# Optimization experiments

Measured on AMD Instinct MI355X. Metric: run time of the kernel, lower is better.

## Reference

```python
import jax, jax.numpy as jnp
import numpy as np

N_LAYERS = 3
HIDDEN = 128
N_NODES = 50000
N_EDGES = 800000
NEG_SLOPE = 0.2  # PyG GATConv default negative_slope
EPS = 1e-16      # PyG softmax denominator eps


def setup_inputs() -> dict:
    key = jax.random.key(0)
    ks = jax.random.split(key, 6)
    z = jax.random.normal(ks[0], (N_NODES, HIDDEN), dtype=jnp.float32)
    edge_index = jax.random.randint(ks[1], (2, N_EDGES), 0, N_NODES, dtype=jnp.int32)
    scale = 1.0 / np.sqrt(HIDDEN)
    Ws = jax.random.normal(ks[2], (N_LAYERS, HIDDEN, HIDDEN), dtype=jnp.float32) * scale
    a_src = jax.random.normal(ks[3], (N_LAYERS, HIDDEN), dtype=jnp.float32) * scale
    a_dst = jax.random.normal(ks[4], (N_LAYERS, HIDDEN), dtype=jnp.float32) * scale
    bias = jnp.zeros((N_LAYERS, HIDDEN), dtype=jnp.float32)
    return {"z": z, "edge_index": edge_index, "Ws": Ws, "a_src": a_src,
            "a_dst": a_dst, "bias": bias}


def _gat_conv(h, W, a_s, a_d, b, src, dst):
    # Linear transform: [N, D]
    x = h @ W
    # Per-node attention logits, gathered per edge
    alpha_s = x @ a_s  # [N]
    alpha_d = x @ a_d  # [N]
    e = jax.nn.leaky_relu(alpha_s[src] + alpha_d[dst], NEG_SLOPE)  # [E]
    # Segment softmax over incoming edges of each destination node
    e_max = jax.ops.segment_max(e, dst, num_segments=N_NODES)
    ex = jnp.exp(e - e_max[dst])
    denom = jax.ops.segment_sum(ex, dst, num_segments=N_NODES)
    alpha = ex / (denom[dst] + EPS)  # [E]
    # Weighted scatter-aggregation of source features
    out = jax.ops.segment_sum(x[src] * alpha[:, None], dst, num_segments=N_NODES)
    return out + b


def reference(z, edge_index, Ws, a_src, a_dst, bias):
    # add_self_loops=True (PyG GATConv default)
    loop = jnp.arange(N_NODES, dtype=edge_index.dtype)
    src = jnp.concatenate([edge_index[0], loop])
    dst = jnp.concatenate([edge_index[1], loop])
    h = z
    for l in range(N_LAYERS):
        h = _gat_conv(h, Ws[l], a_src[l], a_dst[l], bias[l], src, dst)
        if l < N_LAYERS - 1:
            h = jax.nn.relu(h)
    return h
```

## Files before the change

### kernel.cpp

```cpp
#include <hip/hip_runtime.h>

#define NN 50000
#define HID 128
#define NE 800000
#define ET (NE + NN)
#define NEG_SLOPE 0.2f
#define CAP 64

typedef __attribute__((ext_vector_type(8))) short short8v;
typedef __attribute__((ext_vector_type(4))) float f32x4;

__device__ inline float b2f(unsigned short u) {
    union { unsigned int i; float f; } x; x.i = ((unsigned int)u) << 16; return x.f;
}
__device__ inline unsigned short f2b(float f) {
    unsigned int x; __builtin_memcpy(&x, &f, 4);
    unsigned int lsb = (x >> 16) & 1u;
    x += 0x7fffu + lsb;
    return (unsigned short)(x >> 16);
}
__device__ inline void splitbf(float v, unsigned short& hi, unsigned short& lo) {
    hi = f2b(v);
    lo = f2b(v - b2f(hi));
}

__global__ void probe_dtype(const unsigned short* __restrict__ z, int* __restrict__ flag) {
    int lane = threadIdx.x;
    unsigned short a = z[lane * 4];
    unsigned short b = z[lane * 4 + 2];
    int ea = (a >> 7) & 0xFF, eb = (b >> 7) & 0xFF;
    int w1 = (ea >= 0x9A || (ea <= 0x30 && a != 0)) ? 1 : 0;
    int w2 = (eb >= 0x9A || (eb <= 0x30 && b != 0)) ? 1 : 0;
    int wild = __popcll(__ballot(w1)) + __popcll(__ballot(w2));
    if (lane == 0) *flag = (wild < 8) ? 1 : 0;
}

__global__ void cvt3(const void* __restrict__ a, const void* __restrict__ b,
                     const void* __restrict__ c, float* __restrict__ oa,
                     float* __restrict__ ob, float* __restrict__ oc,
                     const int* __restrict__ flag) {
    int i = blockIdx.x * 256 + threadIdx.x;
    if (i >= 3 * 3 * HID) return;
    int which = i / (3 * HID), j = i - which * (3 * HID);
    const void* in = which == 0 ? a : which == 1 ? b : c;
    float* out = which == 0 ? oa : which == 1 ? ob : oc;
    out[j] = *flag ? b2f(((const unsigned short*)in)[j]) : ((const float*)in)[j];
}

__global__ void wprep(const void* __restrict__ Ws, unsigned short* __restrict__ Wb,
                      const int* __restrict__ flag) {
    int i = blockIdx.x * 256 + threadIdx.x;
    if (i >= 3 * HID * HID) return;
    int L = i >> 14;
    int k = (i >> 7) & 127;
    int n = i & 127;
    float v = *flag ? b2f(((const unsigned short*)Ws)[i]) : ((const float*)Ws)[i];
    unsigned short hi, lo;
    splitbf(v, hi, lo);
    unsigned short* hbase = Wb + (size_t)L * 2 * HID * HID;
    unsigned short* lbase = hbase + HID * HID;
    int bo = (n * 256 + k * 2) ^ ((n & 7) << 4);
    *(unsigned short*)((char*)hbase + bo) = hi;
    lbase[n * HID + k] = lo;
}

#define SCHUNK 1024
__global__ __launch_bounds__(256) void scatter_padded(
        const int* __restrict__ ei, int* __restrict__ pos, int* __restrict__ csr) {
    const int rng  = blockIdx.x & 7;
    const int base = (blockIdx.x >> 3) * SCHUNK;
#pragma unroll
    for (int k = 0; k < SCHUNK / 256; ++k) {
        int e = base + k * 256 + threadIdx.x;
        if (e >= ET) continue;
        int d = (e < NE) ? ei[NE + e] : (e - NE);
        if ((d * 8) / NN != rng) continue;
        int s = (e < NE) ? ei[e] : d;
        int slot = atomicAdd(&pos[d], 1);
        if (slot < CAP) csr[(d << 6) + slot] = s;
    }
}

__global__ __launch_bounds__(256) void gemm_alpha(
        const void* __restrict__ h_, const unsigned short* __restrict__ Wb,
        const float* __restrict__ a_s, const float* __restrict__ a_d,
        unsigned short* __restrict__ x, float* __restrict__ alpha_s, float* __restrict__ alpha_d,
        const int* __restrict__ flag) {
    __shared__ unsigned short Wh[HID * HID];
    const int t = threadIdx.x;
    const int base = blockIdx.x * 64;
    const int hf = *flag;
    const unsigned short* Wlo = Wb + HID * HID;

#pragma unroll
    for (int i = 0; i < 8; ++i) {
        int c = i * 256 + t;
        ((short8v*)Wh)[c] = ((const short8v*)Wb)[c];
    }
    __syncthreads();

    const int w  = t >> 6;
    const int l  = t & 63;
    const int lr = l & 15;
    const int lk = l >> 4;
    const int arow = base + w * 16 + lr;
    const bool rowok = (arow < NN);

    const short8v zv = (short8v){0, 0, 0, 0, 0, 0, 0, 0};
    short8v ahi[4], alo[4];
    if (hf) {
        const unsigned short* hp = (const unsigned short*)h_ + (size_t)arow * HID + lk * 8;
#pragma unroll
        for (int ks = 0; ks < 4; ++ks) {
            ahi[ks] = rowok ? *(const short8v*)(hp + ks * 32) : zv;
            alo[ks] = zv;
        }
    } else {
        const float* hp = (const float*)h_ + (size_t)arow * HID + lk * 8;
#pragma unroll
        for (int ks = 0; ks < 4; ++ks) {
            float4 v0 = make_float4(0.f, 0.f, 0.f, 0.f), v1 = v0;
            if (rowok) {
                v0 = *(const float4*)(hp + ks * 32);
                v1 = *(const float4*)(hp + ks * 32 + 4);
            }
            ushort4 h0, l0, h1, l1;
            splitbf(v0.x, h0.x, l0.x); splitbf(v0.y, h0.y, l0.y);
            splitbf(v0.z, h0.z, l0.z); splitbf(v0.w, h0.w, l0.w);
            splitbf(v1.x, h1.x, l1.x); splitbf(v1.y, h1.y, l1.y);
            splitbf(v1.z, h1.z, l1.z); splitbf(v1.w, h1.w, l1.w);
            ahi[ks] = (short8v){(short)h0.x, (short)h0.y, (short)h0.z, (short)h0.w,
                                (short)h1.x, (short)h1.y, (short)h1.z, (short)h1.w};
            alo[ks] = (short8v){(short)l0.x, (short)l0.y, (short)l0.z, (short)l0.w,
                                (short)l1.x, (short)l1.y, (short)l1.z, (short)l1.w};
        }
    }

    f32x4 acc[8];
#pragma unroll
    for (int nt = 0; nt < 8; ++nt) acc[nt] = (f32x4){0.f, 0.f, 0.f, 0.f};

    if (hf) {
#pragma unroll
        for (int ks = 0; ks < 4; ++ks) {
#pragma unroll
            for (int nt = 0; nt < 8; ++nt) {
                int row = nt * 16 + lr;
                int bo = (row * 256 + ks * 64 + lk * 16) ^ ((lr & 7) << 4);
                short8v bhi = *(const short8v*)((const char*)Wh + bo);
                short8v blo = *(const short8v*)(Wlo + row * HID + ks * 32 + lk * 8);
                acc[nt] = __builtin_amdgcn_mfma_f32_16x16x32_bf16(ahi[ks], bhi, acc[nt], 0, 0, 0);
                acc[nt] = __builtin_amdgcn_mfma_f32_16x16x32_bf16(ahi[ks], blo, acc[nt], 0, 0, 0);
            }
        }
    } else {
#pragma unroll
        for (int ks = 0; ks < 4; ++ks) {
#pragma unroll
            for (int nt = 0; nt < 8; ++nt) {
                int row = nt * 16 + lr;
                int bo = (row * 256 + ks * 64 + lk * 16) ^ ((lr & 7) << 4);
                short8v bhi = *(const short8v*)((const char*)Wh + bo);
                short8v blo = *(const short8v*)(Wlo + row * HID + ks * 32 + lk * 8);
                acc[nt] = __builtin_amdgcn_mfma_f32_16x16x32_bf16(ahi[ks], bhi, acc[nt], 0, 0, 0);
                acc[nt] = __builtin_amdgcn_mfma_f32_16x16x32_bf16(alo[ks], bhi, acc[nt], 0, 0, 0);
                acc[nt] = __builtin_amdgcn_mfma_f32_16x16x32_bf16(ahi[ks], blo, acc[nt], 0, 0, 0);
            }
        }
    }

    float ps[4] = {0.f, 0.f, 0.f, 0.f};
    float pd[4] = {0.f, 0.f, 0.f, 0.f};
#pragma unroll
    for (int nt = 0; nt < 8; ++nt) {
        float asv = a_s[nt * 16 + lr];
        float adv = a_d[nt * 16 + lr];
#pragma unroll
        for (int r = 0; r < 4; ++r) {
            ps[r] = fmaf(acc[nt][r], asv, ps[r]);
            pd[r] = fmaf(acc[nt][r], adv, pd[r]);
        }
    }
#pragma unroll
    for (int m = 8; m >= 1; m >>= 1) {
#pragma unroll
        for (int r = 0; r < 4; ++r) {
            ps[r] += __shfl_xor(ps[r], m, 16);
            pd[r] += __shfl_xor(pd[r], m, 16);
        }
    }
#pragma unroll
    for (int r = 0; r < 4; ++r) {
        int grow = base + w * 16 + lk * 4 + r;
        if (grow < NN) {
#pragma unroll
            for (int nt = 0; nt < 8; ++nt)
                x[(size_t)grow * HID + nt * 16 + lr] = f2b(acc[nt][r]);
            if (lr == 0) { alpha_s[grow] = ps[r]; alpha_d[grow] = pd[r]; }
        }
    }
}

__global__ __launch_bounds__(256) void aggregate_fused(
        const unsigned short* __restrict__ x, const int* __restrict__ deg_,
        const int* __restrict__ csr, const float* __restrict__ als,
        const float* __restrict__ ald, const float* __restrict__ bias,
        void* __restrict__ out, const int* __restrict__ flag, int do_relu) {
    int node = (blockIdx.x * 256 + threadIdx.x) >> 6;
    int lane = threadIdx.x & 63;
    if (node >= NN) return;
    int deg = min(deg_[node], CAP);
    const int* list = csr + (node << 6);
    const unsigned int* x2 = (const unsigned int*)x;
    float adv = ald[node];
    float accx = 0.f, accy = 0.f, den = 0.f;
    for (int j0 = 0; j0 < deg; j0 += 8) {
        int idx[8];
#pragma unroll
        for (int k = 0; k < 8; ++k) {
            int j = j0 + k;
            idx[k] = list[j < deg ? j : j0];
        }
        float e8[8];
#pragma unroll
        for (int k = 0; k < 8; ++k) e8[k] = als[idx[k]];
        unsigned int u[8];
#pragma unroll
        for (int k = 0; k < 8; ++k) u[k] = x2[(size_t)idx[k] * 64 + lane];
#pragma unroll
        for (int k = 0; k < 8; ++k) {
            float e = e8[k] + adv;
            e = fmaxf(e, NEG_SLOPE * e);
            e = fminf(e, 60.f);
            float p = (j0 + k < deg) ? __expf(e) : 0.f;
            den += p;
            accx = fmaf(p, b2f((unsigned short)(u[k] & 0xFFFFu)), accx);
            accy = fmaf(p, b2f((unsigned short)(u[k] >> 16)), accy);
        }
    }
    float inv = 1.f / (den + 1e-16f);
    float2 bv = ((const float2*)bias)[lane];
    float ox = accx * inv + bv.x;
    float oy = accy * inv + bv.y;
    if (do_relu) { ox = fmaxf(ox, 0.f); oy = fmaxf(oy, 0.f); }
    if (*flag) {
        ushort2 pk; pk.x = f2b(ox); pk.y = f2b(oy);
        *(ushort2*)((unsigned short*)out + node * HID + lane * 2) = pk;
    } else {
        ((float2*)out)[node * 64 + lane] = make_float2(ox, oy);
    }
}

extern "C" void kernel_launch(void* const* d_in, const int* in_sizes, int n_in,
                              void* d_out, int out_size, void* d_ws, size_t ws_size,
                              hipStream_t stream) {
    const void* z_in  = d_in[0];
    const int*  ei    = (const int*)d_in[1];
    const void* Ws_in = d_in[2];
    const void* as_in = d_in[3];
    const void* ad_in = d_in[4];
    const void* b_in  = d_in[5];

    char* wsp = (char*)d_ws;
    auto alloc = [&](size_t bytes) -> char* {
        char* p = wsp; wsp += (bytes + 255) & ~(size_t)255; return p;
    };
    int*            dflag   = (int*)alloc(4);
    int*            pos     = (int*)alloc(NN * 4);
    int*            csrp    = (int*)alloc((size_t)NN * CAP * 4);
    float*          alpha_s = (float*)alloc(NN * 4);
    float*          alpha_d = (float*)alloc(NN * 4);
    unsigned short* Wb      = (unsigned short*)alloc((size_t)3 * 2 * HID * HID * 2);
    float*          asf     = (float*)alloc(3 * HID * 4);
    float*          adf     = (float*)alloc(3 * HID * 4);
    float*          bff     = (float*)alloc(3 * HID * 4);
    unsigned short* xb      = (unsigned short*)alloc((size_t)NN * HID * 2);

    probe_dtype<<<1, 64, 0, stream>>>((const unsigned short*)z_in, dflag);

    wprep<<<(3 * HID * HID + 255) / 256, 256, 0, stream>>>(Ws_in, Wb, dflag);
    cvt3<<<5, 256, 0, stream>>>(as_in, ad_in, b_in, asf, adf, bff, dflag);

    hipMemsetAsync(pos, 0, NN * 4, stream);
    const int chunks = (ET + SCHUNK - 1) / SCHUNK;
    scatter_padded<<<chunks * 8, 256, 0, stream>>>(ei, pos, csrp);

    const int gemm_blocks = (NN + 63) / 64;
    const int wave_blocks = (NN + 3) / 4;
    const size_t WL = 2 * HID * HID;

    gemm_alpha<<<gemm_blocks, 256, 0, stream>>>(z_in, Wb, asf, adf, xb, alpha_s, alpha_d, dflag);
    aggregate_fused<<<wave_blocks, 256, 0, stream>>>(xb, pos, csrp, alpha_s, alpha_d, bff, d_out, dflag, 1);

    gemm_alpha<<<gemm_blocks, 256, 0, stream>>>(d_out, Wb + WL, asf + HID, adf + HID,
                                                xb, alpha_s, alpha_d, dflag);
    aggregate_fused<<<wave_blocks, 256, 0, stream>>>(xb, pos, csrp, alpha_s, alpha_d, bff + HID, d_out, dflag, 1);

    gemm_alpha<<<gemm_blocks, 256, 0, stream>>>(d_out, Wb + 2 * WL, asf + 2 * HID,
                                                adf + 2 * HID, xb, alpha_s, alpha_d, dflag);
    aggregate_fused<<<wave_blocks, 256, 0, stream>>>(xb, pos, csrp, alpha_s, alpha_d, bff + 2 * HID, d_out, dflag, 0);
}
```

Measured before the change: 313.2 us.

## Split features into column quarters for cache-resident aggregation; fuse prep kernels

The GEMM now writes x in four column-quarter planes of 32 features each. Aggregation runs four passes, one per plane, with each wave handling 4 neighbors in parallel (16 lanes per neighbor) and reducing with shuffles. The goal is to keep each plane's gather working set (about 3.2 MB) in cache and reduce random gather traffic, at the cost of re-reading the CSR and alpha data four times. Separately, the probe, weight conversion, vector conversion and memset are merged into one prep kernel to cut launch overhead.

```diff
diff --git a/kernel.cpp b/kernel.cpp
--- a/kernel.cpp
+++ b/kernel.cpp
@@ -6,6 +6,9 @@
 #define ET (NE + NN)
 #define NEG_SLOPE 0.2f
 #define CAP 64
+#define WTOT (3 * HID * HID)
+#define VTOT (3 * 3 * HID)
+#define NB4  (NN / 4)
 
 typedef __attribute__((ext_vector_type(8))) short short8v;
 typedef __attribute__((ext_vector_type(4))) float f32x4;
@@ -24,44 +27,47 @@
     lo = f2b(v - b2f(hi));
 }
 
-__global__ void probe_dtype(const unsigned short* __restrict__ z, int* __restrict__ flag) {
-    int lane = threadIdx.x;
-    unsigned short a = z[lane * 4];
-    unsigned short b = z[lane * 4 + 2];
-    int ea = (a >> 7) & 0xFF, eb = (b >> 7) & 0xFF;
-    int w1 = (ea >= 0x9A || (ea <= 0x30 && a != 0)) ? 1 : 0;
-    int w2 = (eb >= 0x9A || (eb <= 0x30 && b != 0)) ? 1 : 0;
-    int wild = __popcll(__ballot(w1)) + __popcll(__ballot(w2));
-    if (lane == 0) *flag = (wild < 8) ? 1 : 0;
-}
-
-__global__ void cvt3(const void* __restrict__ a, const void* __restrict__ b,
-                     const void* __restrict__ c, float* __restrict__ oa,
-                     float* __restrict__ ob, float* __restrict__ oc,
-                     const int* __restrict__ flag) {
-    int i = blockIdx.x * 256 + threadIdx.x;
-    if (i >= 3 * 3 * HID) return;
-    int which = i / (3 * HID), j = i - which * (3 * HID);
-    const void* in = which == 0 ? a : which == 1 ? b : c;
-    float* out = which == 0 ? oa : which == 1 ? ob : oc;
-    out[j] = *flag ? b2f(((const unsigned short*)in)[j]) : ((const float*)in)[j];
-}
-
-__global__ void wprep(const void* __restrict__ Ws, unsigned short* __restrict__ Wb,
-                      const int* __restrict__ flag) {
-    int i = blockIdx.x * 256 + threadIdx.x;
-    if (i >= 3 * HID * HID) return;
-    int L = i >> 14;
-    int k = (i >> 7) & 127;
-    int n = i & 127;
-    float v = *flag ? b2f(((const unsigned short*)Ws)[i]) : ((const float*)Ws)[i];
-    unsigned short hi, lo;
-    splitbf(v, hi, lo);
-    unsigned short* hbase = Wb + (size_t)L * 2 * HID * HID;
-    unsigned short* lbase = hbase + HID * HID;
-    int bo = (n * 256 + k * 2) ^ ((n & 7) << 4);
-    *(unsigned short*)((char*)hbase + bo) = hi;
-    lbase[n * HID + k] = lo;
+__global__ __launch_bounds__(256) void prep(
+        const unsigned short* __restrict__ z, const void* __restrict__ Ws,
+        const void* __restrict__ as_, const void* __restrict__ ad_,
+        const void* __restrict__ b_, unsigned short* __restrict__ Wb,
+        float* __restrict__ asf, float* __restrict__ adf, float* __restrict__ bff,
+        int* __restrict__ pos, int* __restrict__ flag) {
+    __shared__ int sflag;
+    const int t = threadIdx.x;
+    if (t < 64) {
+        unsigned short a = z[t * 4];
+        unsigned short b = z[t * 4 + 2];
+        int ea = (a >> 7) & 0xFF, eb = (b >> 7) & 0xFF;
+        int w1 = (ea >= 0x9A || (ea <= 0x30 && a != 0)) ? 1 : 0;
+        int w2 = (eb >= 0x9A || (eb <= 0x30 && b != 0)) ? 1 : 0;
+        int wild = __popcll(__ballot(w1)) + __popcll(__ballot(w2));
+        if (t == 0) sflag = (wild < 8) ? 1 : 0;
+    }
+    __syncthreads();
+    const int f = sflag;
+    const int gtid = blockIdx.x * 256 + t;
+    if (gtid == 0) *flag = f;
+    if (gtid < NN) pos[gtid] = 0;
+    if (gtid < WTOT) {
+        int L = gtid >> 14, k = (gtid >> 7) & 127, n = gtid & 127;
+        float v = f ? b2f(((const unsigned short*)Ws)[gtid]) : ((const float*)Ws)[gtid];
+        unsigned short hi, lo;
+        splitbf(v, hi, lo);
+        unsigned short* hbase = Wb + (size_t)L * 2 * HID * HID;
+        unsigned short* lbase = hbase + HID * HID;
+        int bo = (n * 256 + k * 2) ^ ((n & 7) << 4);
+        *(unsigned short*)((char*)hbase + bo) = hi;
+        lbase[n * HID + k] = lo;
+    } else {
+        int i = gtid - WTOT;
+        if (i < VTOT) {
+            int which = i / (3 * HID), j = i - which * (3 * HID);
+            const void* in = which == 0 ? as_ : which == 1 ? ad_ : b_;
+            float* o = which == 0 ? asf : which == 1 ? adf : bff;
+            o[j] = f ? b2f(((const unsigned short*)in)[j]) : ((const float*)in)[j];
+        }
+    }
 }
 
 #define SCHUNK 1024
@@ -195,59 +201,66 @@
         if (grow < NN) {
 #pragma unroll
             for (int nt = 0; nt < 8; ++nt)
-                x[(size_t)grow * HID + nt * 16 + lr] = f2b(acc[nt][r]);
+                x[(size_t)(nt >> 1) * (NN * 32) + (size_t)grow * 32 + (nt & 1) * 16 + lr]
+                    = f2b(acc[nt][r]);
             if (lr == 0) { alpha_s[grow] = ps[r]; alpha_d[grow] = pd[r]; }
         }
     }
 }
 
-__global__ __launch_bounds__(256) void aggregate_fused(
-        const unsigned short* __restrict__ x, const int* __restrict__ deg_,
+__global__ __launch_bounds__(256) void aggregate_q(
+        const unsigned short* __restrict__ xq, const int* __restrict__ deg_,
         const int* __restrict__ csr, const float* __restrict__ als,
         const float* __restrict__ ald, const float* __restrict__ bias,
         void* __restrict__ out, const int* __restrict__ flag, int do_relu) {
-    int node = (blockIdx.x * 256 + threadIdx.x) >> 6;
-    int lane = threadIdx.x & 63;
-    if (node >= NN) return;
-    int deg = min(deg_[node], CAP);
+    const int pass = blockIdx.x / NB4;
+    const int nb   = blockIdx.x - pass * NB4;
+    const int node = nb * 4 + (threadIdx.x >> 6);
+    const int lane = threadIdx.x & 63;
+    const int g  = lane >> 4;
+    const int cu = lane & 15;
+    const int deg = min(deg_[node], CAP);
     const int* list = csr + (node << 6);
-    const unsigned int* x2 = (const unsigned int*)x;
-    float adv = ald[node];
-    float accx = 0.f, accy = 0.f, den = 0.f;
+    const unsigned int* xs = (const unsigned int*)xq + (size_t)pass * NN * 16;
+    const float adv = ald[node];
+    float ax = 0.f, ay = 0.f, den = 0.f;
     for (int j0 = 0; j0 < deg; j0 += 8) {
-        int idx[8];
-#pragma unroll
-        for (int k = 0; k < 8; ++k) {
-            int j = j0 + k;
-            idx[k] = list[j < deg ? j : j0];
-        }
-        float e8[8];
-#pragma unroll
-        for (int k = 0; k < 8; ++k) e8[k] = als[idx[k]];
-        unsigned int u[8];
-#pragma unroll
-        for (int k = 0; k < 8; ++k) u[k] = x2[(size_t)idx[k] * 64 + lane];
-#pragma unroll
-        for (int k = 0; k < 8; ++k) {
-            float e = e8[k] + adv;
-            e = fmaxf(e, NEG_SLOPE * e);
-            e = fminf(e, 60.f);
-            float p = (j0 + k < deg) ? __expf(e) : 0.f;
-            den += p;
-            accx = fmaf(p, b2f((unsigned short)(u[k] & 0xFFFFu)), accx);
-            accy = fmaf(p, b2f((unsigned short)(u[k] >> 16)), accy);
-        }
-    }
-    float inv = 1.f / (den + 1e-16f);
-    float2 bv = ((const float2*)bias)[lane];
-    float ox = accx * inv + bv.x;
-    float oy = accy * inv + bv.y;
-    if (do_relu) { ox = fmaxf(ox, 0.f); oy = fmaxf(oy, 0.f); }
-    if (*flag) {
-        ushort2 pk; pk.x = f2b(ox); pk.y = f2b(oy);
-        *(ushort2*)((unsigned short*)out + node * HID + lane * 2) = pk;
-    } else {
-        ((float2*)out)[node * 64 + lane] = make_float2(ox, oy);
+        int ja = j0 + g, jb = j0 + 4 + g;
+        int ia = list[ja < deg ? ja : j0];
+        int ib = list[jb < deg ? jb : j0];
+        float ea = als[ia], eb = als[ib];
+        unsigned int ua = xs[(size_t)ia * 16 + cu];
+        unsigned int ub = xs[(size_t)ib * 16 + cu];
+        float e = ea + adv;
+        e = fmaxf(e, NEG_SLOPE * e);
+        e = fminf(e, 60.f);
+        float p = (ja < deg) ? __expf(e) : 0.f;
+        den += p;
+        ax = fmaf(p, b2f((unsigned short)(ua & 0xFFFFu)), ax);
+        ay = fmaf(p, b2f((unsigned short)(ua >> 16)), ay);
+        e = eb + adv;
+        e = fmaxf(e, NEG_SLOPE * e);
+        e = fminf(e, 60.f);
+        p = (jb < deg) ? __expf(e) : 0.f;
+        den += p;
+        ax = fmaf(p, b2f((unsigned short)(ub & 0xFFFFu)), ax);
+        ay = fmaf(p, b2f((unsigned short)(ub >> 16)), ay);
+    }
+    ax += __shfl_xor(ax, 16); ay += __shfl_xor(ay, 16); den += __shfl_xor(den, 16);
+    ax += __shfl_xor(ax, 32); ay += __shfl_xor(ay, 32); den += __shfl_xor(den, 32);
+    if (g == 0) {
+        float inv = 1.f / (den + 1e-16f);
+        int col = pass * 32 + cu * 2;
+        float2 bv = *(const float2*)(bias + col);
+        float ox = ax * inv + bv.x;
+        float oy = ay * inv + bv.y;
+        if (do_relu) { ox = fmaxf(ox, 0.f); oy = fmaxf(oy, 0.f); }
+        if (*flag) {
+            ushort2 pk; pk.x = f2b(ox); pk.y = f2b(oy);
+            *(ushort2*)((unsigned short*)out + (size_t)node * HID + col) = pk;
+        } else {
+            *(float2*)((float*)out + (size_t)node * HID + col) = make_float2(ox, oy);
+        }
     }
 }
 
@@ -276,27 +289,24 @@
     float*          bff     = (float*)alloc(3 * HID * 4);
     unsigned short* xb      = (unsigned short*)alloc((size_t)NN * HID * 2);
 
-    probe_dtype<<<1, 64, 0, stream>>>((const unsigned short*)z_in, dflag);
-
-    wprep<<<(3 * HID * HID + 255) / 256, 256, 0, stream>>>(Ws_in, Wb, dflag);
-    cvt3<<<5, 256, 0, stream>>>(as_in, ad_in, b_in, asf, adf, bff, dflag);
-
-    hipMemsetAsync(pos, 0, NN * 4, stream);
+    prep<<<197, 256, 0, stream>>>((const unsigned short*)z_in, Ws_in, as_in, ad_in, b_in,
+                                  Wb, asf, adf, bff, pos, dflag);
+
     const int chunks = (ET + SCHUNK - 1) / SCHUNK;
     scatter_padded<<<chunks * 8, 256, 0, stream>>>(ei, pos, csrp);
 
     const int gemm_blocks = (NN + 63) / 64;
-    const int wave_blocks = (NN + 3) / 4;
+    const int agg_blocks  = NB4 * 4;
     const size_t WL = 2 * HID * HID;
 
     gemm_alpha<<<gemm_blocks, 256, 0, stream>>>(z_in, Wb, asf, adf, xb, alpha_s, alpha_d, dflag);
-    aggregate_fused<<<wave_blocks, 256, 0, stream>>>(xb, pos, csrp, alpha_s, alpha_d, bff, d_out, dflag, 1);
+    aggregate_q<<<agg_blocks, 256, 0, stream>>>(xb, pos, csrp, alpha_s, alpha_d, bff, d_out, dflag, 1);
 
     gemm_alpha<<<gemm_blocks, 256, 0, stream>>>(d_out, Wb + WL, asf + HID, adf + HID,
                                                 xb, alpha_s, alpha_d, dflag);
-    aggregate_fused<<<wave_blocks, 256, 0, stream>>>(xb, pos, csrp, alpha_s, alpha_d, bff + HID, d_out, dflag, 1);
+    aggregate_q<<<agg_blocks, 256, 0, stream>>>(xb, pos, csrp, alpha_s, alpha_d, bff + HID, d_out, dflag, 1);
 
     gemm_alpha<<<gemm_blocks, 256, 0, stream>>>(d_out, Wb + 2 * WL, asf + 2 * HID,
                                                 adf + 2 * HID, xb, alpha_s, alpha_d, dflag);
-    aggregate_fused<<<wave_blocks, 256, 0, stream>>>(xb, pos, csrp, alpha_s, alpha_d, bff + 2 * HID, d_out, dflag, 0);
-}
+    aggregate_q<<<agg_blocks, 256, 0, stream>>>(xb, pos, csrp, alpha_s, alpha_d, bff + 2 * HID, d_out, dflag, 0);
+}
```

Result: slower. 438.6 us (+40.0%).
